# Kernel tuning notes

Measured on AMD Instinct MI355X. Metric: run time of the kernel, lower is better.

## Reference

```python
import jax, jax.numpy as jnp
import numpy as np

EPS = 1e-5
CIN = [3, 24, 48, 96, 192]
COUT = [24, 48, 96, 192, 384]
P = 512
NUM_CLASSES = 101
FC_IN = 384 * 16 * 3 * 3  # 55296


def _poly_layer(x, proj, alpha, gamma, beta):
    # x: (B, C, D, H, W)
    B, C, D, H, W = x.shape
    # im2col: 3x3x3 patches with zero padding 1 -> (B, C*27, D, H, W)
    patches = jax.lax.conv_general_dilated_patches(
        x, filter_shape=(3, 3, 3), window_strides=(1, 1, 1),
        padding=[(1, 1), (1, 1), (1, 1)])
    patches = jnp.moveaxis(patches, 1, -1)  # (B, D, H, W, C*27)
    ws = jnp.einsum('bdhwk,pk->bdhwp', patches, proj)      # projector GEMM
    out = jnp.einsum('bdhwp,po->bdhwo', ws, alpha)         # alpha GEMM
    out = jnp.maximum(1.0 + out, 0.0)                      # clamp(1+x, min=0)
    out = jnp.moveaxis(out, -1, 1)                         # (B, O, D, H, W)
    # MaxPool3d kernel/stride (1,2,2)
    out = jax.lax.reduce_window(out, -jnp.inf, jax.lax.max,
                                (1, 1, 1, 2, 2), (1, 1, 1, 2, 2), 'VALID')
    # BatchNorm3d with batch statistics (train-mode math)
    mean = out.mean(axis=(0, 2, 3, 4), keepdims=True)
    var = out.var(axis=(0, 2, 3, 4), keepdims=True)
    out = (out - mean) * jax.lax.rsqrt(var + EPS)
    out = out * gamma.reshape(1, -1, 1, 1, 1) + beta.reshape(1, -1, 1, 1, 1)
    return out


def setup_inputs() -> dict:
    key = jax.random.key(0)
    keys = jax.random.split(key, 32)
    inp = {'x': jax.random.normal(keys[0], (2, 3, 16, 112, 112), dtype=jnp.float32)}
    ki = 1
    for i in range(5):
        k_feat = CIN[i] * 27
        inp[f'p{i+1}'] = jax.random.normal(keys[ki], (P, k_feat), dtype=jnp.float32) / np.sqrt(k_feat); ki += 1
        inp[f'a{i+1}'] = jax.random.normal(keys[ki], (P, COUT[i]), dtype=jnp.float32) * np.sqrt(2.0 / COUT[i]); ki += 1
        inp[f'g{i+1}'] = jnp.ones((COUT[i],), dtype=jnp.float32)
        inp[f'q{i+1}'] = jnp.zeros((COUT[i],), dtype=jnp.float32)
    inp['w1'] = jax.random.normal(keys[ki], (512, FC_IN), dtype=jnp.float32) * np.sqrt(2.0 / 512); ki += 1
    inp['b1'] = jnp.zeros((512,), dtype=jnp.float32)
    inp['w2'] = jax.random.normal(keys[ki], (256, 512), dtype=jnp.float32) * np.sqrt(2.0 / 256); ki += 1
    inp['b2'] = jnp.zeros((256,), dtype=jnp.float32)
    inp['w3'] = jax.random.normal(keys[ki], (NUM_CLASSES, 256), dtype=jnp.float32) * np.sqrt(2.0 / NUM_CLASSES); ki += 1
    inp['b3'] = jnp.zeros((NUM_CLASSES,), dtype=jnp.float32)
    return inp


def reference(x, p1, a1, g1, q1, p2, a2, g2, q2, p3, a3, g3, q3,
              p4, a4, g4, q4, p5, a5, g5, q5, w1, b1, w2, b2, w3, b3):
    projs = [p1, p2, p3, p4, p5]
    alphas = [a1, a2, a3, a4, a5]
    gammas = [g1, g2, g3, g4, g5]
    betas = [q1, q2, q3, q4, q5]
    h = x
    for i in range(5):
        h = _poly_layer(h, projs[i], alphas[i], gammas[i], betas[i])
    h = h.reshape(h.shape[0], -1)  # (B, 55296)
    h = jax.nn.relu(h @ w1.T + b1)  # dropout = identity (eval)
    h = jax.nn.relu(h @ w2.T + b2)
    logits = h @ w3.T + b3
    return logits
```

## Files before the change

### kernel.cpp

```cpp
#include <hip/hip_runtime.h>

#define EPS_BN 1e-5f

typedef __attribute__((ext_vector_type(8))) short sh8;
typedef __attribute__((ext_vector_type(4))) short sh4;
typedef __attribute__((ext_vector_type(4))) float f32x4;

static const size_t WF_OFF[5] = {0, 1944, 33048, 157464, 655128};
static const size_t PART_OFF = 2645784;
static const size_t PRE_OFF  = 6258456;
static const size_t OUT5_OFF = 8666904;
static const size_t H_OFF    = 8777496;
static const size_t ST_OFF   = 8888088;
static const size_t BNP_OFF  = 8888856;
static const size_t H1_OFF   = 8938008;
static const size_t WS_TOT   = 8939032;
__device__ __align__(256) float g_ws[WS_TOT];

static const size_t XIN_OFF = 0;
static const size_t A1_OFF  = 1871424;
static const size_t A2_OFF  = 4776768;
static const size_t A3_OFF  = 6331968;
static const size_t A4_OFF  = 7216704;
static const size_t AR_TOT  = 7776576;
__device__ __align__(256) unsigned short g_act[AR_TOT];

static const size_t WB_OFF[5] = {0, 4096, 36352, 162304, 659968};
__device__ __align__(256) unsigned short g_wb[2650624];

__device__ inline unsigned short f2bf(float v) {
    unsigned u = __float_as_uint(v);
    return (unsigned short)((u + 0x7fffu + ((u >> 16) & 1u)) >> 16);
}

__global__ __launch_bounds__(256) void init_input(const float* __restrict__ x,
                                                  unsigned short* __restrict__ xp,
                                                  float* __restrict__ bnp,
                                                  int4* __restrict__ zp, int nz)
{
    const int i = blockIdx.x * 256 + threadIdx.x;
    if (i < nz) zp[i] = make_int4(0, 0, 0, 0);
    if (i < 49152) bnp[i] = 0.f;
    if (i >= 2 * 18 * 114 * 114 * 4) return;
    const int c = i & 3;
    int t = i >> 2;
    const int xx = t % 114; t /= 114;
    const int yy = t % 114; t /= 114;
    const int zz = t % 18;
    const int b  = t / 18;
    float v = 0.f;
    if (c < 3 && (unsigned)(zz - 1) < 16u && (unsigned)(yy - 1) < 112u && (unsigned)(xx - 1) < 112u)
        v = x[(((size_t)b * 3 + c) * 16 + (zz - 1)) * 12544 + (yy - 1) * 112 + (xx - 1)];
    xp[i] = f2bf(v);
}

struct FuseArgs {
    const float* proj[5];
    const float* alpha[5];
    float* Wf[5];
    int K[5];
    int CO[5];
    int NT[5];
    int start[6];
};

__global__ __launch_bounds__(256) void fuse_all(FuseArgs a)
{
    __shared__ __align__(16) float sa[16][64];
    __shared__ __align__(16) float sp[16][64];

    int l = 0;
    {
        const int bx = blockIdx.x;
        while (l < 4 && bx >= a.start[l + 1]) ++l;
    }
    const int idx = blockIdx.x - a.start[l];
    const int NT = a.NT[l];
    const int obase = (idx / NT) * 64;
    const int kbase = (idx % NT) * 64;
    const int K = a.K[l], CO = a.CO[l];
    const float* __restrict__ proj  = a.proj[l];
    const float* __restrict__ alpha = a.alpha[l];
    float* __restrict__ Wf = a.Wf[l];

    const int tid = threadIdx.x;
    const int tk = tid & 15, to = tid >> 4;

    const int pp  = tid >> 4;
    const int col = (tid & 15) * 4;
    const int o_st = obase + col;
    const int k_st = kbase + col;
    const bool a_ok  = (o_st < CO);
    const bool p_vec = ((K & 3) == 0) && (k_st + 4 <= K);

    float acc[4][4];
    #pragma unroll
    for (int i = 0; i < 4; ++i)
        #pragma unroll
        for (int j = 0; j < 4; ++j) acc[i][j] = 0.f;

    for (int p0 = 0; p0 < 512; p0 += 16) {
        const float* ap  = alpha + (size_t)(p0 + pp) * CO;
        const float* prp = proj  + (size_t)(p0 + pp) * K;
        float4 va = make_float4(0.f, 0.f, 0.f, 0.f);
        float4 vp = make_float4(0.f, 0.f, 0.f, 0.f);
        if (a_ok) va = *(const float4*)(ap + o_st);
        if (p_vec) {
            vp = *(const float4*)(prp + k_st);
        } else {
            float t4[4];
            #pragma unroll
            for (int j = 0; j < 4; ++j)
                t4[j] = (k_st + j < K) ? prp[k_st + j] : 0.f;
            vp = make_float4(t4[0], t4[1], t4[2], t4[3]);
        }
        *(float4*)&sa[pp][col] = va;
        *(float4*)&sp[pp][col] = vp;
        __syncthreads();
        #pragma unroll
        for (int p = 0; p < 16; ++p) {
            const float4 a4 = *(const float4*)&sa[p][to * 4];
            const float4 b4 = *(const float4*)&sp[p][tk * 4];
            const float aa[4] = {a4.x, a4.y, a4.z, a4.w};
            const float bb[4] = {b4.x, b4.y, b4.z, b4.w};
            #pragma unroll
            for (int i = 0; i < 4; ++i)
                #pragma unroll
                for (int j = 0; j < 4; ++j)
                    acc[i][j] = fmaf(aa[i], bb[j], acc[i][j]);
        }
        __syncthreads();
    }

    #pragma unroll
    for (int i = 0; i < 4; ++i) {
        const int o = obase + to * 4 + i;
        if (o < CO) {
            #pragma unroll
            for (int j = 0; j < 4; ++j) {
                const int kk = kbase + tk * 4 + j;
                if (kk < K) Wf[(size_t)o * K + kk] = acc[i][j];
            }
        }
    }
}

struct ReordArgs {
    const float* Wf[5];
    unsigned short* Wb[5];
    int K[5], CPAD[5], KPAD[5], CO[5];
    int start[6];
};

__global__ __launch_bounds__(256) void reorder_all(ReordArgs a)
{
    int l = 0;
    {
        const int bx = blockIdx.x;
        while (l < 4 && bx >= a.start[l + 1]) ++l;
    }
    const int o = blockIdx.x - a.start[l];
    const int K = a.K[l], CPAD = a.CPAD[l], KPAD = a.KPAD[l], CO = a.CO[l];
    const int tid = threadIdx.x;
    unsigned short* row = a.Wb[l] + (size_t)o * KPAD;
    for (int i = tid; i < KPAD; i += 256) row[i] = 0;
    __syncthreads();
    if (o < CO) {
        const float* wr = a.Wf[l] + (size_t)o * K;
        for (int k = tid; k < K; k += 256) {
            const int c = k / 27, s = k - c * 27;
            row[s * CPAD + c] = f2bf(wr[k]);
        }
    }
}

template<int CPAD, int COUT, int KPAD, int HI, int WI, int HP, int WP, int NBLK, int SPLIT>
__global__ __launch_bounds__(256) void conv_mfma(
    const unsigned short* __restrict__ in, const unsigned short* __restrict__ Wb,
    float* __restrict__ outf, float* __restrict__ part, float* __restrict__ bnp)
{
    constexpr int NT = NBLK / 16;
    constexpr int HI2 = HI + 2, WI2 = WI + 2;
    constexpr bool C8 = (CPAD % 8 == 0);
    constexpr int TABN = C8 ? KPAD / 8 : KPAD / 4;
    constexpr int NSTEP = KPAD / 32 / SPLIT;
    constexpr int MTOT = 2 * 16 * HP * WP * 4;
    constexpr bool BONCE = (NBLK * KPAD * 2 <= 16384);
    constexpr int BROW = BONCE ? (KPAD + 8) : 40;
    constexpr int BS_ELEMS = BONCE ? NBLK * BROW : 2 * NBLK * 40;

    __shared__ __align__(16) unsigned short As[2][64 * 40];
    __shared__ __align__(16) unsigned short Bs[BS_ELEMS];
    __shared__ int tab[TABN];
    __shared__ float bs[(SPLIT == 1) ? 2 * NBLK : 1];

    const int tid = threadIdx.x;
    const int lane = tid & 63;
    const int wv = tid >> 6;
    const int blk_m = blockIdx.x;
    const int oc0 = blockIdx.y * NBLK;
    const int kc = (SPLIT > 1) ? blockIdx.z : 0;

    for (int i = tid; i < TABN; i += 256) {
        const int k = i * (C8 ? 8 : 4);
        const int s = k / CPAD, c = k % CPAD;
        tab[i] = (s < 27) ? ((((s / 9) * HI2 + (s % 9) / 3) * WI2 + (s % 3)) * CPAD + c) : -1;
    }

    if constexpr (BONCE) {
        for (int i = tid; i < NBLK * KPAD / 8; i += 256) {
            const int r = i / (KPAD / 8), kk = i - r * (KPAD / 8);
            *(sh8*)&Bs[r * BROW + kk * 8] = *(const sh8*)&Wb[(size_t)(oc0 + r) * KPAD + kk * 8];
        }
    }

    const int m_l = tid & 63;
    const int oct = tid >> 6;
    const int m_g = blk_m * 64 + m_l;
    const int pooled = m_g >> 2, sub = m_g & 3;
    const int pw_g = pooled % WP;
    const int ph_g = (pooled / WP) % HP;
    const int d_g  = (pooled / (WP * HP)) & 15;
    const int b_g  = pooled / (WP * HP * 16);
    const int h_g = 2 * ph_g + (sub >> 1);
    const int w_g = 2 * pw_g + (sub & 1);
    const size_t base_m = ((((size_t)b_g * 18 + d_g) * HI2 + h_g) * WI2 + w_g) * CPAD;

    const int brow = tid >> 2, bcc = tid & 3;
    const bool bload = (tid < NBLK * 4);

    f32x4 acc[NT];
    #pragma unroll
    for (int i = 0; i < NT; ++i) acc[i] = (f32x4){0.f, 0.f, 0.f, 0.f};

    const int k_begin = kc * NSTEP * 32;

    sh8 aA; sh4 a0r, a1r; sh8 brg;

    __syncthreads();

    {
        const int k0 = k_begin;
        if constexpr (C8) {
            const int off = tab[(k0 >> 3) + oct];
            aA = (sh8){0, 0, 0, 0, 0, 0, 0, 0};
            if (off >= 0) aA = *(const sh8*)(in + base_m + off);
            *(sh8*)&As[0][m_l * 40 + oct * 8] = aA;
        } else {
            const int o0 = tab[(k0 >> 2) + oct * 2];
            const int o1 = tab[(k0 >> 2) + oct * 2 + 1];
            a0r = (sh4){0, 0, 0, 0}; a1r = (sh4){0, 0, 0, 0};
            if (o0 >= 0) a0r = *(const sh4*)(in + base_m + o0);
            if (o1 >= 0) a1r = *(const sh4*)(in + base_m + o1);
            *(sh4*)&As[0][m_l * 40 + oct * 8]     = a0r;
            *(sh4*)&As[0][m_l * 40 + oct * 8 + 4] = a1r;
        }
        if constexpr (!BONCE) {
            if (bload) {
                brg = *(const sh8*)&Wb[(size_t)(oc0 + brow) * KPAD + k0 + bcc * 8];
                *(sh8*)&Bs[0 + brow * 40 + bcc * 8] = brg;
            }
        }
    }
    __syncthreads();

    int cur = 0;
    for (int s = 0; s < NSTEP; ++s) {
        const int k0 = k_begin + s * 32;
        if (s + 1 < NSTEP) {
            const int kn = k0 + 32;
            if constexpr (C8) {
                const int off = tab[(kn >> 3) + oct];
                aA = (sh8){0, 0, 0, 0, 0, 0, 0, 0};
                if (off >= 0) aA = *(const sh8*)(in + base_m + off);
            } else {
                const int o0 = tab[(kn >> 2) + oct * 2];
                const int o1 = tab[(kn >> 2) + oct * 2 + 1];
                a0r = (sh4){0, 0, 0, 0}; a1r = (sh4){0, 0, 0, 0};
                if (o0 >= 0) a0r = *(const sh4*)(in + base_m + o0);
                if (o1 >= 0) a1r = *(const sh4*)(in + base_m + o1);
            }
            if constexpr (!BONCE) {
                if (bload) brg = *(const sh8*)&Wb[(size_t)(oc0 + brow) * KPAD + kn + bcc * 8];
            }
        }
        const sh8 af = *(const sh8*)&As[cur][(wv * 16 + (lane & 15)) * 40 + (lane >> 4) * 8];
        #pragma unroll
        for (int nt = 0; nt < NT; ++nt) {
            sh8 bf;
            if constexpr (BONCE)
                bf = *(const sh8*)&Bs[(nt * 16 + (lane & 15)) * BROW + k0 + (lane >> 4) * 8];
            else
                bf = *(const sh8*)&Bs[cur * NBLK * 40 + (nt * 16 + (lane & 15)) * 40 + (lane >> 4) * 8];
            acc[nt] = __builtin_amdgcn_mfma_f32_16x16x32_bf16(af, bf, acc[nt], 0, 0, 0);
        }
        if (s + 1 < NSTEP) {
            if constexpr (C8) {
                *(sh8*)&As[cur ^ 1][m_l * 40 + oct * 8] = aA;
            } else {
                *(sh4*)&As[cur ^ 1][m_l * 40 + oct * 8]     = a0r;
                *(sh4*)&As[cur ^ 1][m_l * 40 + oct * 8 + 4] = a1r;
            }
            if constexpr (!BONCE) {
                if (bload) *(sh8*)&Bs[(cur ^ 1) * NBLK * 40 + brow * 40 + bcc * 8] = brg;
            }
        }
        __syncthreads();
        cur ^= 1;
    }

    const int q = lane >> 4;
    const int nloc = lane & 15;
    if constexpr (SPLIT == 1) {
        for (int i = tid; i < 2 * NBLK; i += 256) bs[i] = 0.f;
        __syncthreads();
        const int pooled_o = blk_m * 16 + wv * 4 + q;
        #pragma unroll
        for (int nt = 0; nt < NT; ++nt) {
            const int oc = oc0 + nt * 16 + nloc;
            float mx = fmaxf(1.f + acc[nt][0], 0.f);
            mx = fmaxf(mx, fmaxf(1.f + acc[nt][1], 0.f));
            mx = fmaxf(mx, fmaxf(1.f + acc[nt][2], 0.f));
            mx = fmaxf(mx, fmaxf(1.f + acc[nt][3], 0.f));
            float s1 = 0.f;
            if (oc < COUT) {
                outf[(size_t)pooled_o * COUT + oc] = mx;
                s1 = mx;
            }
            float s2 = s1 * s1;
            s1 += __shfl_xor(s1, 16);
            s1 += __shfl_xor(s1, 32);
            s2 += __shfl_xor(s2, 16);
            s2 += __shfl_xor(s2, 32);
            if (q == 0) {
                atomicAdd(&bs[nt * 16 + nloc], s1);
                atomicAdd(&bs[NBLK + nt * 16 + nloc], s2);
            }
        }
        __syncthreads();
        float* rowp = bnp + (size_t)(blk_m & 63) * 768;
        for (int i = tid; i < NBLK; i += 256) {
            const int oc = oc0 + i;
            if (oc < COUT) {
                atomicAdd(&rowp[oc], bs[i]);
                atomicAdd(&rowp[384 + oc], bs[NBLK + i]);
            }
        }
    } else {
        #pragma unroll
        for (int nt = 0; nt < NT; ++nt) {
            const int oc = oc0 + nt * 16 + nloc;
            #pragma unroll
            for (int r = 0; r < 4; ++r) {
                const int mm = blk_m * 64 + wv * 16 + q * 4 + r;
                part[((size_t)kc * MTOT + mm) * COUT + oc] = acc[nt][r];
            }
        }
    }
}

template<int COUT, int HP, int WP, int SPLIT>
__global__ __launch_bounds__(256) void pool_epi(const float* __restrict__ part,
                                                float* __restrict__ outf,
                                                float* __restrict__ bnp)
{
    constexpr int PO = 2 * 16 * HP * WP;
    constexpr int M = PO * 4;
    __shared__ float bs[2 * COUT];
    const int tid = threadIdx.x;
    for (int i = tid; i < 2 * COUT; i += 256) bs[i] = 0.f;
    __syncthreads();
    const int idx = blockIdx.x * 256 + tid;
    if (idx < PO * COUT) {
        const int oc = idx % COUT;
        const int p = idx / COUT;
        float v[4] = {0.f, 0.f, 0.f, 0.f};
        for (int s = 0; s < SPLIT; ++s)
            #pragma unroll
            for (int r = 0; r < 4; ++r)
                v[r] += part[((size_t)s * M + p * 4 + r) * COUT + oc];
        float mx = fmaxf(1.f + v[0], 0.f);
        mx = fmaxf(mx, fmaxf(1.f + v[1], 0.f));
        mx = fmaxf(mx, fmaxf(1.f + v[2], 0.f));
        mx = fmaxf(mx, fmaxf(1.f + v[3], 0.f));
        outf[(size_t)p * COUT + oc] = mx;
        atomicAdd(&bs[oc], mx);
        atomicAdd(&bs[COUT + oc], mx * mx);
    }
    __syncthreads();
    float* rowp = bnp + (size_t)(blockIdx.x & 63) * 768;
    for (int i = tid; i < COUT; i += 256) {
        atomicAdd(&rowp[i], bs[i]);
        atomicAdd(&rowp[384 + i], bs[COUT + i]);
    }
}

__global__ __launch_bounds__(64) void bn_reduce(float* __restrict__ bnp,
                                                const float* __restrict__ gamma,
                                                const float* __restrict__ beta,
                                                float* __restrict__ st,
                                                float inv_n)
{
    const int c = blockIdx.x, tid = threadIdx.x;
    float s = bnp[(size_t)tid * 768 + c];
    float q = bnp[(size_t)tid * 768 + 384 + c];
    bnp[(size_t)tid * 768 + c] = 0.f;
    bnp[(size_t)tid * 768 + 384 + c] = 0.f;
    #pragma unroll
    for (int off = 32; off > 0; off >>= 1) {
        s += __shfl_down(s, off);
        q += __shfl_down(q, off);
    }
    if (tid == 0) {
        const float mean = s * inv_n;
        const float var  = q * inv_n - mean * mean;
        const float sc   = gamma[c] * rsqrtf(var + EPS_BN);
        st[2 * c]     = sc;
        st[2 * c + 1] = fmaf(-mean, sc, beta[c]);
    }
}

template<int C, int HP, int WP>
__global__ __launch_bounds__(256) void bn_apply_halo(const float* __restrict__ pre,
                                                     const float* __restrict__ st,
                                                     unsigned short* __restrict__ outh)
{
    constexpr int PO = 2 * 16 * HP * WP;
    const int idx = blockIdx.x * 256 + threadIdx.x;
    if (idx >= PO * C) return;
    const int c = idx % C;
    const int p = idx / C;
    const int pw = p % WP;
    const int ph = (p / WP) % HP;
    const int d  = (p / (WP * HP)) & 15;
    const int b  = p / (WP * HP * 16);
    const float v = fmaf(pre[idx], st[2 * c], st[2 * c + 1]);
    outh[((((size_t)b * 18 + d + 1) * (HP + 2) + ph + 1) * (WP + 2) + pw + 1) * C + c] = f2bf(v);
}

__global__ __launch_bounds__(256) void transpose5(const float* __restrict__ out5,
                                                  const float* __restrict__ st,
                                                  float* __restrict__ h)
{
    const int idx = blockIdx.x * 256 + threadIdx.x;
    if (idx >= 110592) return;
    const int c = idx % 384;
    const int p = idx / 384;
    const int b = p / 144;
    const int sp = p % 144;
    h[(size_t)b * 55296 + c * 144 + sp] = fmaf(out5[idx], st[2 * c], st[2 * c + 1]);
}

__global__ __launch_bounds__(256) void fc1_k(const float* __restrict__ h,
                                             const float* __restrict__ w1,
                                             const float* __restrict__ b1,
                                             float* __restrict__ hout)
{
    __shared__ float r0[256];
    __shared__ float r1[256];
    const int j = blockIdx.x, tid = threadIdx.x;
    const float* wr = w1 + (size_t)j * 55296;
    float a0 = 0.f, a1 = 0.f;
    for (int k = tid * 4; k < 55296; k += 1024) {
        const float4 w = *(const float4*)(wr + k);
        const float4 u = *(const float4*)(h + k);
        const float4 v = *(const float4*)(h + 55296 + k);
        a0 += w.x * u.x + w.y * u.y + w.z * u.z + w.w * u.w;
        a1 += w.x * v.x + w.y * v.y + w.z * v.z + w.w * v.w;
    }
    r0[tid] = a0; r1[tid] = a1;
    __syncthreads();
    for (int off = 128; off > 0; off >>= 1) {
        if (tid < off) { r0[tid] += r0[tid + off]; r1[tid] += r1[tid + off]; }
        __syncthreads();
    }
    if (tid == 0) {
        hout[j]       = fmaxf(r0[0] + b1[j], 0.f);
        hout[512 + j] = fmaxf(r1[0] + b1[j], 0.f);
    }
}

__global__ __launch_bounds__(256) void fc23_k(const float* __restrict__ h1,
                                              const float* __restrict__ w2,
                                              const float* __restrict__ b2,
                                              const float* __restrict__ w3,
                                              const float* __restrict__ b3,
                                              float* __restrict__ out)
{
    __shared__ float h1s[1024];
    __shared__ float h2[512];
    const int tid = threadIdx.x;
    for (int i = tid; i < 1024; i += 256) h1s[i] = h1[i];
    __syncthreads();
    {
        const float* wr = w2 + (size_t)tid * 512;
        #pragma unroll
        for (int b = 0; b < 2; ++b) {
            float a = 0.f;
            const float* hh = h1s + b * 512;
            for (int k = 0; k < 512; ++k) a = fmaf(wr[k], hh[k], a);
            h2[b * 256 + tid] = fmaxf(a + b2[tid], 0.f);
        }
    }
    __syncthreads();
    if (tid < 101) {
        const float* wr = w3 + (size_t)tid * 256;
        #pragma unroll
        for (int b = 0; b < 2; ++b) {
            float a = 0.f;
            const float* hh = h2 + b * 256;
            for (int k = 0; k < 256; ++k) a = fmaf(wr[k], hh[k], a);
            out[b * 101 + tid] = a + b3[tid];
        }
    }
}

extern "C" void kernel_launch(void* const* d_in, const int* in_sizes, int n_in,
                              void* d_out, int out_size, void* d_ws, size_t ws_size,
                              hipStream_t stream)
{
    const float* x  = (const float*)d_in[0];
    const float* p[5], *al[5], *g[5], *q[5];
    for (int i = 0; i < 5; ++i) {
        p[i]  = (const float*)d_in[1 + 4 * i];
        al[i] = (const float*)d_in[2 + 4 * i];
        g[i]  = (const float*)d_in[3 + 4 * i];
        q[i]  = (const float*)d_in[4 + 4 * i];
    }
    const float* w1 = (const float*)d_in[21];
    const float* b1 = (const float*)d_in[22];
    const float* w2 = (const float*)d_in[23];
    const float* b2 = (const float*)d_in[24];
    const float* w3 = (const float*)d_in[25];
    const float* b3 = (const float*)d_in[26];

    float* ws = nullptr;
    hipGetSymbolAddress((void**)&ws, HIP_SYMBOL(g_ws));
    unsigned short* act = nullptr;
    hipGetSymbolAddress((void**)&act, HIP_SYMBOL(g_act));
    unsigned short* wb = nullptr;
    hipGetSymbolAddress((void**)&wb, HIP_SYMBOL(g_wb));

    float* Wf[5];
    for (int i = 0; i < 5; ++i) Wf[i] = ws + WF_OFF[i];
    float* part = ws + PART_OFF;
    float* pre  = ws + PRE_OFF;
    float* out5 = ws + OUT5_OFF;
    float* h    = ws + H_OFF;
    float* st   = ws + ST_OFF;
    float* bnp  = ws + BNP_OFF;
    float* h1   = ws + H1_OFF;

    unsigned short* xin = act + XIN_OFF;
    unsigned short* a1  = act + A1_OFF;
    unsigned short* a2  = act + A2_OFF;
    unsigned short* a3  = act + A3_OFF;
    unsigned short* a4  = act + A4_OFF;

    {
        const int nz = (int)((AR_TOT - A1_OFF) * 2 / 16);
        init_input<<<(2 * 18 * 114 * 114 * 4 + 255) / 256, 256, 0, stream>>>(
            x, xin, bnp, (int4*)(act + A1_OFF), nz);
    }

    static const int KF[5] = {81, 648, 1296, 2592, 5184};
    static const int CO[5] = {24, 48, 96, 192, 384};
    static const int CP[5] = {4, 24, 48, 96, 192};
    static const int KP[5] = {128, 672, 1312, 2592, 5184};
    static const int NPAD[5] = {32, 48, 96, 192, 384};

    FuseArgs fa;
    int s0 = 0;
    for (int i = 0; i < 5; ++i) {
        fa.proj[i] = p[i]; fa.alpha[i] = al[i]; fa.Wf[i] = Wf[i];
        fa.K[i] = KF[i]; fa.CO[i] = CO[i];
        const int nt = (KF[i] + 63) / 64;
        const int mt = (CO[i] + 63) / 64;
        fa.NT[i] = nt;
        fa.start[i] = s0;
        s0 += nt * mt;
    }
    fa.start[5] = s0;
    fuse_all<<<s0, 256, 0, stream>>>(fa);

    ReordArgs ra;
    int r0 = 0;
    for (int i = 0; i < 5; ++i) {
        ra.Wf[i] = Wf[i]; ra.Wb[i] = wb + WB_OFF[i];
        ra.K[i] = KF[i]; ra.CPAD[i] = CP[i]; ra.KPAD[i] = KP[i]; ra.CO[i] = CO[i];
        ra.start[i] = r0;
        r0 += NPAD[i];
    }
    ra.start[5] = r0;
    reorder_all<<<r0, 256, 0, stream>>>(ra);

    conv_mfma<4, 24, 128, 112, 112, 56, 56, 32, 1>
        <<<dim3(6272, 1), 256, 0, stream>>>(xin, wb + WB_OFF[0], pre, nullptr, bnp);
    bn_reduce<<<24, 64, 0, stream>>>(bnp, g[0], q[0], st, 1.f / 100352.f);
    bn_apply_halo<24, 56, 56><<<9408, 256, 0, stream>>>(pre, st, a1);

    conv_mfma<24, 48, 672, 56, 56, 28, 28, 48, 1>
        <<<dim3(1568, 1), 256, 0, stream>>>(a1, wb + WB_OFF[1], pre, nullptr, bnp);
    bn_reduce<<<48, 64, 0, stream>>>(bnp, g[1], q[1], st, 1.f / 25088.f);
    bn_apply_halo<48, 28, 28><<<4704, 256, 0, stream>>>(pre, st, a2);

    conv_mfma<48, 96, 1312, 28, 28, 14, 14, 48, 1>
        <<<dim3(392, 2), 256, 0, stream>>>(a2, wb + WB_OFF[2], pre, nullptr, bnp);
    bn_reduce<<<96, 64, 0, stream>>>(bnp, g[2], q[2], st, 1.f / 6272.f);
    bn_apply_halo<96, 14, 14><<<2352, 256, 0, stream>>>(pre, st, a3);

    conv_mfma<96, 192, 2592, 14, 14, 7, 7, 64, 3>
        <<<dim3(98, 3, 3), 256, 0, stream>>>(a3, wb + WB_OFF[3], nullptr, part, bnp);
    pool_epi<192, 7, 7, 3><<<1176, 256, 0, stream>>>(part, pre, bnp);
    bn_reduce<<<192, 64, 0, stream>>>(bnp, g[3], q[3], st, 1.f / 1568.f);
    bn_apply_halo<192, 7, 7><<<1176, 256, 0, stream>>>(pre, st, a4);

    conv_mfma<192, 384, 5184, 7, 7, 3, 3, 64, 6>
        <<<dim3(18, 6, 6), 256, 0, stream>>>(a4, wb + WB_OFF[4], nullptr, part, bnp);
    pool_epi<384, 3, 3, 6><<<432, 256, 0, stream>>>(part, out5, bnp);
    bn_reduce<<<384, 64, 0, stream>>>(bnp, g[4], q[4], st, 1.f / 288.f);

    transpose5<<<(110592 + 255) / 256, 256, 0, stream>>>(out5, st, h);
    fc1_k<<<512, 256, 0, stream>>>(h, w1, b1, h1);
    fc23_k<<<1, 256, 0, stream>>>(h1, w2, b2, w3, b3, (float*)d_out);
}
```

Baseline: 511.5 us.

## Double the conv GEMM M-tile to 128 rows per block with two MFMA fragments

Each conv_mfma block now computes 128 output rows instead of 64. Each wave issues two MFMAs per B fragment, so every B load from LDS is reused twice, and the launch grids are halved. Each thread now loads twice as many im2col elements. The goal is fewer LDS B reads per MFMA and less per-block setup such as the weight preload and tab construction. The cost is more registers, more LDS for the A tile, and fewer blocks, which hurts the small layers 4 and 5 (e.g. 9x6x6 blocks).

```diff
diff --git a/kernel.cpp b/kernel.cpp
--- a/kernel.cpp
+++ b/kernel.cpp
@@ -189,7 +189,7 @@
     constexpr int BROW = BONCE ? (KPAD + 8) : 40;
     constexpr int BS_ELEMS = BONCE ? NBLK * BROW : 2 * NBLK * 40;
 
-    __shared__ __align__(16) unsigned short As[2][64 * 40];
+    __shared__ __align__(16) unsigned short As[2][128 * 40];
     __shared__ __align__(16) unsigned short Bs[BS_ELEMS];
     __shared__ int tab[TABN];
     __shared__ float bs[(SPLIT == 1) ? 2 * NBLK : 1];
@@ -214,46 +214,63 @@
         }
     }
 
-    const int m_l = tid & 63;
-    const int oct = tid >> 6;
-    const int m_g = blk_m * 64 + m_l;
-    const int pooled = m_g >> 2, sub = m_g & 3;
-    const int pw_g = pooled % WP;
-    const int ph_g = (pooled / WP) % HP;
-    const int d_g  = (pooled / (WP * HP)) & 15;
-    const int b_g  = pooled / (WP * HP * 16);
-    const int h_g = 2 * ph_g + (sub >> 1);
-    const int w_g = 2 * pw_g + (sub & 1);
+    const int srow = tid >> 1;
+    const int half = tid & 1;
+    const int m_g = blk_m * 128 + srow;
+    {
+    }
+    const int pooled_s = m_g >> 2, sub_s = m_g & 3;
+    const int pw_g = pooled_s % WP;
+    const int ph_g = (pooled_s / WP) % HP;
+    const int d_g  = (pooled_s / (WP * HP)) & 15;
+    const int b_g  = pooled_s / (WP * HP * 16);
+    const int h_g = 2 * ph_g + (sub_s >> 1);
+    const int w_g = 2 * pw_g + (sub_s & 1);
     const size_t base_m = ((((size_t)b_g * 18 + d_g) * HI2 + h_g) * WI2 + w_g) * CPAD;
 
     const int brow = tid >> 2, bcc = tid & 3;
     const bool bload = (tid < NBLK * 4);
 
-    f32x4 acc[NT];
+    f32x4 acc[2][NT];
     #pragma unroll
-    for (int i = 0; i < NT; ++i) acc[i] = (f32x4){0.f, 0.f, 0.f, 0.f};
+    for (int mf = 0; mf < 2; ++mf)
+        #pragma unroll
+        for (int i = 0; i < NT; ++i) acc[mf][i] = (f32x4){0.f, 0.f, 0.f, 0.f};
 
     const int k_begin = kc * NSTEP * 32;
 
-    sh8 aA; sh4 a0r, a1r; sh8 brg;
+    sh8 aA0, aA1;
+    sh4 aP0, aP1, aP2, aP3;
+    sh8 brg;
 
     __syncthreads();
 
     {
         const int k0 = k_begin;
         if constexpr (C8) {
-            const int off = tab[(k0 >> 3) + oct];
-            aA = (sh8){0, 0, 0, 0, 0, 0, 0, 0};
-            if (off >= 0) aA = *(const sh8*)(in + base_m + off);
-            *(sh8*)&As[0][m_l * 40 + oct * 8] = aA;
+            const int o0 = tab[(k0 >> 3) + half * 2];
+            const int o1 = tab[(k0 >> 3) + half * 2 + 1];
+            aA0 = (sh8){0, 0, 0, 0, 0, 0, 0, 0};
+            aA1 = (sh8){0, 0, 0, 0, 0, 0, 0, 0};
+            if (o0 >= 0) aA0 = *(const sh8*)(in + base_m + o0);
+            if (o1 >= 0) aA1 = *(const sh8*)(in + base_m + o1);
+            *(sh8*)&As[0][srow * 40 + (half * 2) * 8]     = aA0;
+            *(sh8*)&As[0][srow * 40 + (half * 2 + 1) * 8] = aA1;
         } else {
-            const int o0 = tab[(k0 >> 2) + oct * 2];
-            const int o1 = tab[(k0 >> 2) + oct * 2 + 1];
-            a0r = (sh4){0, 0, 0, 0}; a1r = (sh4){0, 0, 0, 0};
-            if (o0 >= 0) a0r = *(const sh4*)(in + base_m + o0);
-            if (o1 >= 0) a1r = *(const sh4*)(in + base_m + o1);
-            *(sh4*)&As[0][m_l * 40 + oct * 8]     = a0r;
-            *(sh4*)&As[0][m_l * 40 + oct * 8 + 4] = a1r;
+            const int t0 = tab[(k0 >> 2) + half * 4];
+            const int t1 = tab[(k0 >> 2) + half * 4 + 1];
+            const int t2 = tab[(k0 >> 2) + half * 4 + 2];
+            const int t3 = tab[(k0 >> 2) + half * 4 + 3];
+            aP0 = (sh4){0, 0, 0, 0}; aP1 = (sh4){0, 0, 0, 0};
+            aP2 = (sh4){0, 0, 0, 0}; aP3 = (sh4){0, 0, 0, 0};
+            if (t0 >= 0) aP0 = *(const sh4*)(in + base_m + t0);
+            if (t1 >= 0) aP1 = *(const sh4*)(in + base_m + t1);
+            if (t2 >= 0) aP2 = *(const sh4*)(in + base_m + t2);
+            if (t3 >= 0) aP3 = *(const sh4*)(in + base_m + t3);
+            *(sh4*)&As[0][srow * 40 + (half * 4) * 4]     = aP0;
+            *(sh4*)&As[0][srow * 40 + (half * 4 + 1) * 4] = aP1;
+            *(sh4*)&As[0][srow * 40 + (half * 4 + 2) * 4] = aP2;
+            *(sh4*)&As[0][srow * 40 + (half * 4 + 3) * 4] = aP3;
         }
         if constexpr (!BONCE) {
             if (bload) {
@@ -270,21 +287,30 @@
         if (s + 1 < NSTEP) {
             const int kn = k0 + 32;
             if constexpr (C8) {
-                const int off = tab[(kn >> 3) + oct];
-                aA = (sh8){0, 0, 0, 0, 0, 0, 0, 0};
-                if (off >= 0) aA = *(const sh8*)(in + base_m + off);
+                const int o0 = tab[(kn >> 3) + half * 2];
+                const int o1 = tab[(kn >> 3) + half * 2 + 1];
+                aA0 = (sh8){0, 0, 0, 0, 0, 0, 0, 0};
+                aA1 = (sh8){0, 0, 0, 0, 0, 0, 0, 0};
+                if (o0 >= 0) aA0 = *(const sh8*)(in + base_m + o0);
+                if (o1 >= 0) aA1 = *(const sh8*)(in + base_m + o1);
             } else {
-                const int o0 = tab[(kn >> 2) + oct * 2];
-                const int o1 = tab[(kn >> 2) + oct * 2 + 1];
-                a0r = (sh4){0, 0, 0, 0}; a1r = (sh4){0, 0, 0, 0};
-                if (o0 >= 0) a0r = *(const sh4*)(in + base_m + o0);
-                if (o1 >= 0) a1r = *(const sh4*)(in + base_m + o1);
+                const int t0 = tab[(kn >> 2) + half * 4];
+                const int t1 = tab[(kn >> 2) + half * 4 + 1];
+                const int t2 = tab[(kn >> 2) + half * 4 + 2];
+                const int t3 = tab[(kn >> 2) + half * 4 + 3];
+                aP0 = (sh4){0, 0, 0, 0}; aP1 = (sh4){0, 0, 0, 0};
+                aP2 = (sh4){0, 0, 0, 0}; aP3 = (sh4){0, 0, 0, 0};
+                if (t0 >= 0) aP0 = *(const sh4*)(in + base_m + t0);
+                if (t1 >= 0) aP1 = *(const sh4*)(in + base_m + t1);
+                if (t2 >= 0) aP2 = *(const sh4*)(in + base_m + t2);
+                if (t3 >= 0) aP3 = *(const sh4*)(in + base_m + t3);
             }
             if constexpr (!BONCE) {
                 if (bload) brg = *(const sh8*)&Wb[(size_t)(oc0 + brow) * KPAD + kn + bcc * 8];
             }
         }
-        const sh8 af = *(const sh8*)&As[cur][(wv * 16 + (lane & 15)) * 40 + (lane >> 4) * 8];
+        const sh8 af0 = *(const sh8*)&As[cur][(wv * 16 + (lane & 15)) * 40 + (lane >> 4) * 8];
+        const sh8 af1 = *(const sh8*)&As[cur][(64 + wv * 16 + (lane & 15)) * 40 + (lane >> 4) * 8];
         #pragma unroll
         for (int nt = 0; nt < NT; ++nt) {
             sh8 bf;
@@ -292,14 +318,18 @@
                 bf = *(const sh8*)&Bs[(nt * 16 + (lane & 15)) * BROW + k0 + (lane >> 4) * 8];
             else
                 bf = *(const sh8*)&Bs[cur * NBLK * 40 + (nt * 16 + (lane & 15)) * 40 + (lane >> 4) * 8];
-            acc[nt] = __builtin_amdgcn_mfma_f32_16x16x32_bf16(af, bf, acc[nt], 0, 0, 0);
+            acc[0][nt] = __builtin_amdgcn_mfma_f32_16x16x32_bf16(af0, bf, acc[0][nt], 0, 0, 0);
+            acc[1][nt] = __builtin_amdgcn_mfma_f32_16x16x32_bf16(af1, bf, acc[1][nt], 0, 0, 0);
         }
         if (s + 1 < NSTEP) {
             if constexpr (C8) {
-                *(sh8*)&As[cur ^ 1][m_l * 40 + oct * 8] = aA;
+                *(sh8*)&As[cur ^ 1][srow * 40 + (half * 2) * 8]     = aA0;
+                *(sh8*)&As[cur ^ 1][srow * 40 + (half * 2 + 1) * 8] = aA1;
             } else {
-                *(sh4*)&As[cur ^ 1][m_l * 40 + oct * 8]     = a0r;
-                *(sh4*)&As[cur ^ 1][m_l * 40 + oct * 8 + 4] = a1r;
+                *(sh4*)&As[cur ^ 1][srow * 40 + (half * 4) * 4]     = aP0;
+                *(sh4*)&As[cur ^ 1][srow * 40 + (half * 4 + 1) * 4] = aP1;
+                *(sh4*)&As[cur ^ 1][srow * 40 + (half * 4 + 2) * 4] = aP2;
+                *(sh4*)&As[cur ^ 1][srow * 40 + (half * 4 + 3) * 4] = aP3;
             }
             if constexpr (!BONCE) {
                 if (bload) *(sh8*)&Bs[(cur ^ 1) * NBLK * 40 + brow * 40 + bcc * 8] = brg;
@@ -314,27 +344,30 @@
     if constexpr (SPLIT == 1) {
         for (int i = tid; i < 2 * NBLK; i += 256) bs[i] = 0.f;
         __syncthreads();
-        const int pooled_o = blk_m * 16 + wv * 4 + q;
-        #pragma unroll
-        for (int nt = 0; nt < NT; ++nt) {
-            const int oc = oc0 + nt * 16 + nloc;
-            float mx = fmaxf(1.f + acc[nt][0], 0.f);
-            mx = fmaxf(mx, fmaxf(1.f + acc[nt][1], 0.f));
-            mx = fmaxf(mx, fmaxf(1.f + acc[nt][2], 0.f));
-            mx = fmaxf(mx, fmaxf(1.f + acc[nt][3], 0.f));
-            float s1 = 0.f;
-            if (oc < COUT) {
-                outf[(size_t)pooled_o * COUT + oc] = mx;
-                s1 = mx;
-            }
-            float s2 = s1 * s1;
-            s1 += __shfl_xor(s1, 16);
-            s1 += __shfl_xor(s1, 32);
-            s2 += __shfl_xor(s2, 16);
-            s2 += __shfl_xor(s2, 32);
-            if (q == 0) {
-                atomicAdd(&bs[nt * 16 + nloc], s1);
-                atomicAdd(&bs[NBLK + nt * 16 + nloc], s2);
+        #pragma unroll
+        for (int mf = 0; mf < 2; ++mf) {
+            const int pooled_o = blk_m * 32 + mf * 16 + wv * 4 + q;
+            #pragma unroll
+            for (int nt = 0; nt < NT; ++nt) {
+                const int oc = oc0 + nt * 16 + nloc;
+                float mx = fmaxf(1.f + acc[mf][nt][0], 0.f);
+                mx = fmaxf(mx, fmaxf(1.f + acc[mf][nt][1], 0.f));
+                mx = fmaxf(mx, fmaxf(1.f + acc[mf][nt][2], 0.f));
+                mx = fmaxf(mx, fmaxf(1.f + acc[mf][nt][3], 0.f));
+                float s1 = 0.f;
+                if (oc < COUT) {
+                    outf[(size_t)pooled_o * COUT + oc] = mx;
+                    s1 = mx;
+                }
+                float s2 = s1 * s1;
+                s1 += __shfl_xor(s1, 16);
+                s1 += __shfl_xor(s1, 32);
+                s2 += __shfl_xor(s2, 16);
+                s2 += __shfl_xor(s2, 32);
+                if (q == 0) {
+                    atomicAdd(&bs[nt * 16 + nloc], s1);
+                    atomicAdd(&bs[NBLK + nt * 16 + nloc], s2);
+                }
             }
         }
         __syncthreads();
@@ -348,12 +381,15 @@
         }
     } else {
         #pragma unroll
-        for (int nt = 0; nt < NT; ++nt) {
-            const int oc = oc0 + nt * 16 + nloc;
+        for (int mf = 0; mf < 2; ++mf) {
             #pragma unroll
-            for (int r = 0; r < 4; ++r) {
-                const int mm = blk_m * 64 + wv * 16 + q * 4 + r;
-                part[((size_t)kc * MTOT + mm) * COUT + oc] = acc[nt][r];
+            for (int nt = 0; nt < NT; ++nt) {
+                const int oc = oc0 + nt * 16 + nloc;
+                #pragma unroll
+                for (int r = 0; r < 4; ++r) {
+                    const int mm = blk_m * 128 + mf * 64 + wv * 16 + q * 4 + r;
+                    part[((size_t)kc * MTOT + mm) * COUT + oc] = acc[mf][nt][r];
+                }
             }
         }
     }
@@ -595,28 +631,28 @@
     reorder_all<<<r0, 256, 0, stream>>>(ra);
 
     conv_mfma<4, 24, 128, 112, 112, 56, 56, 32, 1>
-        <<<dim3(6272, 1), 256, 0, stream>>>(xin, wb + WB_OFF[0], pre, nullptr, bnp);
+        <<<dim3(3136, 1), 256, 0, stream>>>(xin, wb + WB_OFF[0], pre, nullptr, bnp);
     bn_reduce<<<24, 64, 0, stream>>>(bnp, g[0], q[0], st, 1.f / 100352.f);
     bn_apply_halo<24, 56, 56><<<9408, 256, 0, stream>>>(pre, st, a1);
 
     conv_mfma<24, 48, 672, 56, 56, 28, 28, 48, 1>
-        <<<dim3(1568, 1), 256, 0, stream>>>(a1, wb + WB_OFF[1], pre, nullptr, bnp);
+        <<<dim3(784, 1), 256, 0, stream>>>(a1, wb + WB_OFF[1], pre, nullptr, bnp);
     bn_reduce<<<48, 64, 0, stream>>>(bnp, g[1], q[1], st, 1.f / 25088.f);
     bn_apply_halo<48, 28, 28><<<4704, 256, 0, stream>>>(pre, st, a2);
 
     conv_mfma<48, 96, 1312, 28, 28, 14, 14, 48, 1>
-        <<<dim3(392, 2), 256, 0, stream>>>(a2, wb + WB_OFF[2], pre, nullptr, bnp);
+        <<<dim3(196, 2), 256, 0, stream>>>(a2, wb + WB_OFF[2], pre, nullptr, bnp);
     bn_reduce<<<96, 64, 0, stream>>>(bnp, g[2], q[2], st, 1.f / 6272.f);
     bn_apply_halo<96, 14, 14><<<2352, 256, 0, stream>>>(pre, st, a3);
 
     conv_mfma<96, 192, 2592, 14, 14, 7, 7, 64, 3>
-        <<<dim3(98, 3, 3), 256, 0, stream>>>(a3, wb + WB_OFF[3], nullptr, part, bnp);
+        <<<dim3(49, 3, 3), 256, 0, stream>>>(a3, wb + WB_OFF[3], nullptr, part, bnp);
     pool_epi<192, 7, 7, 3><<<1176, 256, 0, stream>>>(part, pre, bnp);
     bn_reduce<<<192, 64, 0, stream>>>(bnp, g[3], q[3], st, 1.f / 1568.f);
     bn_apply_halo<192, 7, 7><<<1176, 256, 0, stream>>>(pre, st, a4);
 
     conv_mfma<192, 384, 5184, 7, 7, 3, 3, 64, 6>
-        <<<dim3(18, 6, 6), 256, 0, stream>>>(a4, wb + WB_OFF[4], nullptr, part, bnp);
+        <<<dim3(9, 6, 6), 256, 0, stream>>>(a4, wb + WB_OFF[4], nullptr, part, bnp);
     pool_epi<384, 3, 3, 6><<<432, 256, 0, stream>>>(part, out5, bnp);
     bn_reduce<<<384, 64, 0, stream>>>(bnp, g[4], q[4], st, 1.f / 288.f);
 
```

New measurement: 514.0 us. No clear change (+0.5%).
